# Kernel optimization log

Hardware: AMD Instinct MI355X
Metric: run time of the kernel (lower is better)

Reference implementation:

```python
import jax, jax.numpy as jnp
import numpy as np
from jax import lax

SCALE = 2
K_UP = 5
EPS = 1e-5
DN = ('NCHW', 'OIHW', 'NCHW')


def _bn(x, gamma, beta, mean, var):
    inv = gamma / jnp.sqrt(var + EPS)
    return x * inv[None, :, None, None] + (beta - mean * inv)[None, :, None, None]


def _pixel_shuffle(x, r):
    b, crr, h, w = x.shape
    c = crr // (r * r)
    x = x.reshape(b, c, r, r, h, w)
    x = x.transpose(0, 1, 4, 2, 5, 3)  # b, c, h, r, w, r
    return x.reshape(b, c, h * r, w * r)


def setup_inputs() -> dict:
    key = jax.random.key(0)
    ks = jax.random.split(key, 4)
    b, c, h, w = 4, 64, 128, 128
    c_mid = 64
    enc_out = (SCALE * K_UP) ** 2  # 100
    return {
        'X': jax.random.normal(ks[0], (b, c, h, w), jnp.float32),
        'comp_w': jax.random.normal(ks[1], (c_mid, c, 1, 1), jnp.float32) * 0.1,
        'comp_gamma': jnp.ones((c_mid,), jnp.float32),
        'comp_beta': jnp.zeros((c_mid,), jnp.float32),
        'comp_mean': jnp.zeros((c_mid,), jnp.float32),
        'comp_var': jnp.ones((c_mid,), jnp.float32),
        'enc_w': jax.random.normal(ks[2], (enc_out, c_mid, 3, 3), jnp.float32) * 0.05,
        'enc_b': jnp.zeros((enc_out,), jnp.float32),
        'enc_gamma': jnp.ones((enc_out,), jnp.float32),
        'enc_beta': jnp.zeros((enc_out,), jnp.float32),
        'enc_mean': jnp.zeros((enc_out,), jnp.float32),
        'enc_var': jnp.ones((enc_out,), jnp.float32),
    }


def reference(X, comp_w, comp_gamma, comp_beta, comp_mean, comp_var,
              enc_w, enc_b, enc_gamma, enc_beta, enc_mean, enc_var):
    b, c, h, w = X.shape
    h_, w_ = h * SCALE, w * SCALE
    # compress: 1x1 conv + BN + ReLU
    Wm = lax.conv_general_dilated(X, comp_w, (1, 1), 'VALID', dimension_numbers=DN)
    Wm = jax.nn.relu(_bn(Wm, comp_gamma, comp_beta, comp_mean, comp_var))
    # encode kernel weights: 3x3 conv + BN
    Wm = lax.conv_general_dilated(Wm, enc_w, (1, 1), ((1, 1), (1, 1)), dimension_numbers=DN)
    Wm = Wm + enc_b[None, :, None, None]
    Wm = _bn(Wm, enc_gamma, enc_beta, enc_mean, enc_var)
    # pixel shuffle -> [b, k_up^2, h_, w_], softmax over kernel dim
    Wm = _pixel_shuffle(Wm, SCALE)
    Wm = jax.nn.softmax(Wm, axis=1)
    # nearest upsample input
    Xu = jnp.repeat(jnp.repeat(X, SCALE, axis=2), SCALE, axis=3)  # [b,c,h_,w_]
    # unfold(k=5, dilation=2, pad=4) + einsum, fused as accumulation over the
    # 25 kernel taps (avoids the b*c*25*h_*w_ im2col blowup; identical math)
    pad = (K_UP // 2) * SCALE  # 4
    Xp = jnp.pad(Xu, ((0, 0), (0, 0), (pad, pad), (pad, pad)))
    out = jnp.zeros((b, c, h_, w_), X.dtype)
    for i in range(K_UP):
        for j in range(K_UP):
            k = i * K_UP + j
            patch = lax.dynamic_slice(Xp, (0, 0, i * SCALE, j * SCALE), (b, c, h_, w_))
            out = out + Wm[:, k:k + 1] * patch
    return out
```

## Files before the change

kernel.cpp:

```cpp
#include <hip/hip_runtime.h>

#define EPS 1e-5f

typedef __attribute__((ext_vector_type(8))) short short8;
typedef __attribute__((ext_vector_type(4))) float float4v;

__device__ inline unsigned short f2bf(float f) {
  unsigned u = __float_as_uint(f);
  unsigned r = (u + 0x7fffu + ((u >> 16) & 1u)) >> 16;
  return (unsigned short)r;
}
__device__ inline uint pk2(float a, float b) {
  return (uint)f2bf(a) | ((uint)f2bf(b) << 16);
}

__global__ __launch_bounds__(256) void xform_kernel(
    const float* __restrict__ enc_w, const float* __restrict__ enc_gamma,
    const float* __restrict__ enc_var, const float* __restrict__ comp_w,
    const float* __restrict__ comp_gamma, const float* __restrict__ comp_var,
    ushort* __restrict__ Awt, float* __restrict__ Wc) {
  int u = blockIdx.x * 256 + threadIdx.x;
  if (u < 9216) {
    int kc = u >> 9, rem = u & 511;
    int mt = rem >> 6, q = (rem >> 4) & 3, ml = rem & 15;
    int e = mt * 16 + ml;
    int t = kc >> 1, h = kc & 1;
    int dy = t / 3, dx = t - dy * 3;
    float inv = (e < 100) ? enc_gamma[e] * rsqrtf(enc_var[e] + EPS) : 0.f;
    ushort o[8];
#pragma unroll
    for (int j = 0; j < 8; ++j) {
      int ci = h * 32 + q * 8 + j;
      float w = (e < 100) ? enc_w[(e * 64 + ci) * 9 + dy * 3 + dx] * inv : 0.f;
      o[j] = f2bf(w);
    }
    uint4 v;
    v.x = (uint)o[0] | ((uint)o[1] << 16);
    v.y = (uint)o[2] | ((uint)o[3] << 16);
    v.z = (uint)o[4] | ((uint)o[5] << 16);
    v.w = (uint)o[6] | ((uint)o[7] << 16);
    *reinterpret_cast<uint4*>(Awt + (size_t)u * 8) = v;
  } else if (u < 9216 + 4096) {
    int v = u - 9216;
    int co = v & 63;
    float inv = comp_gamma[co] * rsqrtf(comp_var[co] + EPS);
    Wc[v] = comp_w[co * 64 + (v >> 6)] * inv;
  }
}

__global__ void bias_kernel(
    const float* __restrict__ enc_b, const float* __restrict__ enc_gamma,
    const float* __restrict__ enc_beta, const float* __restrict__ enc_mean,
    const float* __restrict__ enc_var, const float* __restrict__ comp_gamma,
    const float* __restrict__ comp_beta, const float* __restrict__ comp_mean,
    const float* __restrict__ comp_var, float* __restrict__ bias2,
    float* __restrict__ bias_c) {
  int t = threadIdx.x;
  if (t < 128) {
    float v = 0.f;
    if (t < 100) {
      float inv = enc_gamma[t] * rsqrtf(enc_var[t] + EPS);
      v = enc_b[t] * inv + enc_beta[t] - enc_mean[t] * inv;
    }
    bias2[t] = v;
  } else if (t < 192) {
    int c = t - 128;
    float inv = comp_gamma[c] * rsqrtf(comp_var[c] + EPS);
    bias_c[c] = comp_beta[c] - comp_mean[c] * inv;
  }
}

__global__ __launch_bounds__(256) void compress_kernel(
    const float* __restrict__ X, const float* __restrict__ Wc,
    const float* __restrict__ bias_c, ushort* __restrict__ out,
    ushort* __restrict__ Xb) {
  __shared__ __align__(16) float xtile[64 * 65];
  __shared__ __align__(16) float osm[64 * 68];
  const int tid = threadIdx.x;
  const int p0 = blockIdx.x * 64;
  const int b = p0 >> 14;
  const float* xbase = X + ((size_t)b << 20) + (p0 & 16383);

#pragma unroll
  for (int k = 0; k < 16; ++k) {
    int u = k * 256 + tid;
    int ci = u >> 6, px = u & 63;
    xtile[px * 65 + ci] = xbase[((size_t)ci << 14) + px];
  }
  __syncthreads();

  const int wv = __builtin_amdgcn_readfirstlane(tid >> 6);
  const int ln = tid & 63;
  float acc[16];
#pragma unroll
  for (int u = 0; u < 16; ++u) acc[u] = bias_c[wv * 16 + u];
  const float* xr = xtile + ln * 65;
#pragma unroll 8
  for (int ci = 0; ci < 64; ++ci) {
    float xv = xr[ci];
    const float* wr = Wc + ci * 64 + wv * 16;
#pragma unroll
    for (int u = 0; u < 16; ++u) acc[u] = fmaf(wr[u], xv, acc[u]);
  }
  float4v* orow = reinterpret_cast<float4v*>(osm) + ln * 17 + wv * 4;
#pragma unroll
  for (int j = 0; j < 4; ++j) {
    float4v t;
#pragma unroll
    for (int s = 0; s < 4; ++s) t[s] = fmaxf(acc[j * 4 + s], 0.f);
    orow[j] = t;
  }
  __syncthreads();

#pragma unroll
  for (int j = 0; j < 2; ++j) {
    int u = j * 256 + tid;
    int px = u >> 3, g = u & 7;
    const float* so = osm + px * 68 + g * 8;
    uint4 vo = make_uint4(pk2(so[0], so[1]), pk2(so[2], so[3]),
                          pk2(so[4], so[5]), pk2(so[6], so[7]));
    *reinterpret_cast<uint4*>(out + (size_t)(p0 + px) * 64 + g * 8) = vo;
    const float* sx = xtile + px * 65 + g * 8;
    uint4 vx = make_uint4(pk2(sx[0], sx[1]), pk2(sx[2], sx[3]),
                          pk2(sx[4], sx[5]), pk2(sx[6], sx[7]));
    *reinterpret_cast<uint4*>(Xb + (size_t)(p0 + px) * 64 + g * 8) = vx;
  }
}

__global__ __launch_bounds__(256) void encode_mfma(
    const ushort* __restrict__ Wm1t, const ushort* __restrict__ Awt,
    const float* __restrict__ bias2, uint* __restrict__ Wtu) {
  __shared__ __align__(16) char smem[25600];
  ushort* Xt = (ushort*)smem;
  const int tid = threadIdx.x;
  const int b = blockIdx.z;
  const int y0 = blockIdx.y * 8, x0 = blockIdx.x * 8;

  for (int u = tid; u < 800; u += 256) {
    int pos = u >> 3, cg = u & 7;
    int iy = pos / 10, ix = pos - iy * 10;
    int gy = y0 + iy - 1, gx = x0 + ix - 1;
    uint4 v = make_uint4(0, 0, 0, 0);
    if ((unsigned)gy < 128u && (unsigned)gx < 128u)
      v = *reinterpret_cast<const uint4*>(
          Wm1t + ((((size_t)b << 14) + (gy << 7) + gx) << 6) + cg * 8);
    *reinterpret_cast<uint4*>(&Xt[pos * 72 + cg * 8]) = v;
  }
  __syncthreads();

  const int wave = tid >> 6, lane = tid & 63;
  const int q = lane >> 4, px16 = lane & 15;

  float4v acc[2][4];
#pragma unroll
  for (int a = 0; a < 2; ++a)
#pragma unroll
    for (int n = 0; n < 4; ++n) acc[a][n] = (float4v){0.f, 0.f, 0.f, 0.f};

  const short8* Ap = reinterpret_cast<const short8*>(Awt);
#pragma unroll
  for (int kc = 0; kc < 18; ++kc) {
    const int t = kc >> 1, h = kc & 1;
    const int dy = t / 3, dx = t - dy * 3;
    short8 af[2];
#pragma unroll
    for (int a = 0; a < 2; ++a)
      af[a] = Ap[kc * 512 + (wave * 2 + a) * 64 + lane];
    short8 bfr[4];
#pragma unroll
    for (int n = 0; n < 4; ++n) {
      int p = n * 16 + px16;
      int iy = (p >> 3) + dy, ix = (p & 7) + dx;
      bfr[n] = *reinterpret_cast<const short8*>(
          &Xt[(iy * 10 + ix) * 72 + h * 32 + q * 8]);
    }
#pragma unroll
    for (int a = 0; a < 2; ++a)
#pragma unroll
      for (int n = 0; n < 4; ++n)
        acc[a][n] = __builtin_amdgcn_mfma_f32_16x16x32_bf16(
            af[a], bfr[n], acc[a][n], 0, 0, 0);
  }
  __syncthreads();

  float* wsm = (float*)smem;
#pragma unroll
  for (int a = 0; a < 2; ++a) {
    int ebase = (wave * 2 + a) * 16 + q * 4;
    if (ebase < 100) {
#pragma unroll
      for (int n = 0; n < 4; ++n) {
        int p = n * 16 + px16;
        *reinterpret_cast<float4v*>(wsm + p * 100 + ebase) = acc[a][n];
      }
    }
  }
  __syncthreads();

  if (tid < 64) {
    const float4v* bias4 = (const float4v*)bias2;
    float4v v[25];
    const float* wp = wsm + tid * 100;
#pragma unroll
    for (int j = 0; j < 25; ++j)
      v[j] = *reinterpret_cast<const float4v*>(wp + 4 * j) + bias4[j];
    float4v m = v[0];
#pragma unroll
    for (int j = 1; j < 25; ++j) {
      m.x = fmaxf(m.x, v[j].x); m.y = fmaxf(m.y, v[j].y);
      m.z = fmaxf(m.z, v[j].z); m.w = fmaxf(m.w, v[j].w);
    }
    float4v s = (float4v){0.f, 0.f, 0.f, 0.f};
#pragma unroll
    for (int j = 0; j < 25; ++j) {
      v[j].x = __expf(v[j].x - m.x); v[j].y = __expf(v[j].y - m.y);
      v[j].z = __expf(v[j].z - m.z); v[j].w = __expf(v[j].w - m.w);
      s += v[j];
    }
    float i0 = 1.f / s.x, i1 = 1.f / s.y, i2 = 1.f / s.z, i3 = 1.f / s.w;
    alignas(16) uint wp56[56];
#pragma unroll
    for (int k = 0; k < 25; ++k) {
      wp56[k]      = (uint)f2bf(v[k].x * i0) | ((uint)f2bf(v[k].y * i1) << 16);
      wp56[28 + k] = (uint)f2bf(v[k].z * i2) | ((uint)f2bf(v[k].w * i3) << 16);
    }
#pragma unroll
    for (int k = 25; k < 28; ++k) { wp56[k] = 0; wp56[28 + k] = 0; }
    int pix = b * 16384 + (y0 + (tid >> 3)) * 128 + x0 + (tid & 7);
    uint4* dst = reinterpret_cast<uint4*>(Wtu + (size_t)pix * 56);
#pragma unroll
    for (int j = 0; j < 14; ++j) dst[j] = reinterpret_cast<const uint4*>(wp56)[j];
  }
}

__global__ __launch_bounds__(256) void carafe_kernel(
    const ushort* __restrict__ Xb, const uint* __restrict__ Wtu,
    float* __restrict__ out) {
  const int tid = threadIdx.x;
  const int b = blockIdx.z;
  const int y0 = blockIdx.y * 8, x0 = blockIdx.x * 8;
  __shared__ __align__(16) ushort xt[144 * 72];

  for (int u = tid; u < 1152; u += 256) {
    int pos = u >> 3, cg = u & 7;
    int iy = pos / 12, ix = pos - iy * 12;
    int gy = y0 + iy - 2, gx = x0 + ix - 2;
    uint4 v = make_uint4(0, 0, 0, 0);
    if ((unsigned)gy < 128u && (unsigned)gx < 128u)
      v = *reinterpret_cast<const uint4*>(
          Xb + (((size_t)b * 16384 + gy * 128 + gx) << 6) + cg * 8);
    *reinterpret_cast<uint4*>(&xt[pos * 72 + cg * 8]) = v;
  }
  __syncthreads();

  const int p = tid & 63, q = tid >> 6;
  const int r1 = q & 1, cq = q >> 1;
  const int py = p >> 3, px = p & 7;

  int pix = b * 16384 + (y0 + py) * 128 + (x0 + px);
  const uint4* wq = reinterpret_cast<const uint4*>(Wtu + (size_t)pix * 56 + r1 * 28);
  alignas(16) uint w[28];
#pragma unroll
  for (int j = 0; j < 7; ++j) reinterpret_cast<uint4*>(w)[j] = wq[j];

  float2 acc[32];
#pragma unroll
  for (int i = 0; i < 32; ++i) acc[i] = make_float2(0.f, 0.f);

#pragma unroll
  for (int k = 0; k < 25; ++k) {
    const int dy = k / 5, dx = k - dy * 5;
    const ushort* bp = xt + ((py + dy) * 12 + (px + dx)) * 72 + cq * 32;
    float w0 = __uint_as_float(w[k] << 16);
    float w1 = __uint_as_float(w[k] & 0xffff0000u);
#pragma unroll
    for (int j = 0; j < 4; ++j) {
      uint4 xv = *reinterpret_cast<const uint4*>(bp + 8 * j);
      const uint xu[4] = {xv.x, xv.y, xv.z, xv.w};
#pragma unroll
      for (int t = 0; t < 4; ++t) {
        float xlo = __uint_as_float(xu[t] << 16);
        float xhi = __uint_as_float(xu[t] & 0xffff0000u);
        int c = j * 8 + t * 2;
        acc[c].x = fmaf(w0, xlo, acc[c].x);
        acc[c].y = fmaf(w1, xlo, acc[c].y);
        acc[c + 1].x = fmaf(w0, xhi, acc[c + 1].x);
        acc[c + 1].y = fmaf(w1, xhi, acc[c + 1].y);
      }
    }
  }

  int yq = (y0 + py) * 2 + r1;
  int xq = (x0 + px) * 2;
#pragma unroll
  for (int ci = 0; ci < 32; ++ci) {
    int c = cq * 32 + ci;
    *reinterpret_cast<float2*>(
        out + ((size_t)(b * 64 + c) * 256 + yq) * 256 + xq) = acc[ci];
  }
}

extern "C" void kernel_launch(void* const* d_in, const int* in_sizes, int n_in,
                              void* d_out, int out_size, void* d_ws, size_t ws_size,
                              hipStream_t stream) {
  const float* X          = (const float*)d_in[0];
  const float* comp_w     = (const float*)d_in[1];
  const float* comp_gamma = (const float*)d_in[2];
  const float* comp_beta  = (const float*)d_in[3];
  const float* comp_mean  = (const float*)d_in[4];
  const float* comp_var   = (const float*)d_in[5];
  const float* enc_w      = (const float*)d_in[6];
  const float* enc_b      = (const float*)d_in[7];
  const float* enc_gamma  = (const float*)d_in[8];
  const float* enc_beta   = (const float*)d_in[9];
  const float* enc_mean   = (const float*)d_in[10];
  const float* enc_var    = (const float*)d_in[11];
  float* out = (float*)d_out;

  char* ws = (char*)d_ws;
  ushort* Wm1t  = (ushort*)(ws);
  uint*   Wtu   = (uint*)(ws + 8388608);
  ushort* Xb    = (ushort*)(ws + 23068672);
  ushort* Awt   = (ushort*)(ws + 31457280);
  float*  Wc    = (float*)(ws + 31604736);
  float*  bias2 = (float*)(ws + 31621120);
  float*  biasc = (float*)(ws + 31621632);

  xform_kernel<<<52, 256, 0, stream>>>(enc_w, enc_gamma, enc_var,
                                       comp_w, comp_gamma, comp_var, Awt, Wc);
  bias_kernel<<<1, 256, 0, stream>>>(enc_b, enc_gamma, enc_beta, enc_mean,
                                     enc_var, comp_gamma, comp_beta, comp_mean,
                                     comp_var, bias2, biasc);
  compress_kernel<<<1024, 256, 0, stream>>>(X, Wc, biasc, Wm1t, Xb);
  encode_mfma<<<dim3(16, 16, 4), 256, 0, stream>>>(Wm1t, Awt, bias2, Wtu);
  carafe_kernel<<<dim3(16, 16, 4), 256, 0, stream>>>(Xb, Wtu, out);
}
```

Measured before the change: 148.1 us.

## Fuse encode and CARAFE kernels and merge bias setup into xform kernel

Merges the encoder MFMA kernel with the CARAFE reassembly kernel. Softmax weights now stay in shared memory instead of being written to and reread from a global buffer. The bias-computation kernel is folded into the weight-transform kernel, which removes a launch. In exchange, the fused kernel uses more shared memory (about 39 KB), which may lower occupancy, and the reassembly phase now runs behind the encode phase inside one block.

```diff
diff --git a/kernel.cpp b/kernel.cpp
--- a/kernel.cpp
+++ b/kernel.cpp
@@ -18,7 +18,11 @@
     const float* __restrict__ enc_w, const float* __restrict__ enc_gamma,
     const float* __restrict__ enc_var, const float* __restrict__ comp_w,
     const float* __restrict__ comp_gamma, const float* __restrict__ comp_var,
-    ushort* __restrict__ Awt, float* __restrict__ Wc) {
+    const float* __restrict__ enc_b, const float* __restrict__ enc_beta,
+    const float* __restrict__ enc_mean, const float* __restrict__ comp_beta,
+    const float* __restrict__ comp_mean, ushort* __restrict__ Awt,
+    float* __restrict__ Wc, float* __restrict__ bias2,
+    float* __restrict__ bias_c) {
   int u = blockIdx.x * 256 + threadIdx.x;
   if (u < 9216) {
     int kc = u >> 9, rem = u & 511;
@@ -40,31 +44,21 @@
     v.z = (uint)o[4] | ((uint)o[5] << 16);
     v.w = (uint)o[6] | ((uint)o[7] << 16);
     *reinterpret_cast<uint4*>(Awt + (size_t)u * 8) = v;
-  } else if (u < 9216 + 4096) {
+  } else if (u < 13312) {
     int v = u - 9216;
     int co = v & 63;
     float inv = comp_gamma[co] * rsqrtf(comp_var[co] + EPS);
     Wc[v] = comp_w[co * 64 + (v >> 6)] * inv;
-  }
-}
-
-__global__ void bias_kernel(
-    const float* __restrict__ enc_b, const float* __restrict__ enc_gamma,
-    const float* __restrict__ enc_beta, const float* __restrict__ enc_mean,
-    const float* __restrict__ enc_var, const float* __restrict__ comp_gamma,
-    const float* __restrict__ comp_beta, const float* __restrict__ comp_mean,
-    const float* __restrict__ comp_var, float* __restrict__ bias2,
-    float* __restrict__ bias_c) {
-  int t = threadIdx.x;
-  if (t < 128) {
+  } else if (u < 13440) {
+    int t = u - 13312;
     float v = 0.f;
     if (t < 100) {
       float inv = enc_gamma[t] * rsqrtf(enc_var[t] + EPS);
       v = enc_b[t] * inv + enc_beta[t] - enc_mean[t] * inv;
     }
     bias2[t] = v;
-  } else if (t < 192) {
-    int c = t - 128;
+  } else if (u < 13504) {
+    int c = u - 13440;
     float inv = comp_gamma[c] * rsqrtf(comp_var[c] + EPS);
     bias_c[c] = comp_beta[c] - comp_mean[c] * inv;
   }
@@ -127,10 +121,11 @@
   }
 }
 
-__global__ __launch_bounds__(256) void encode_mfma(
+__global__ __launch_bounds__(256) void encode_carafe(
     const ushort* __restrict__ Wm1t, const ushort* __restrict__ Awt,
-    const float* __restrict__ bias2, uint* __restrict__ Wtu) {
-  __shared__ __align__(16) char smem[25600];
+    const float* __restrict__ bias2, const ushort* __restrict__ Xb,
+    float* __restrict__ out) {
+  __shared__ __align__(16) char smem[39936];
   ushort* Xt = (ushort*)smem;
   const int tid = threadIdx.x;
   const int b = blockIdx.z;
@@ -197,6 +192,7 @@
   }
   __syncthreads();
 
+  uint* wpT = (uint*)(smem + 25600);
   if (tid < 64) {
     const float4v* bias4 = (const float4v*)bias2;
     float4v v[25];
@@ -218,29 +214,15 @@
       s += v[j];
     }
     float i0 = 1.f / s.x, i1 = 1.f / s.y, i2 = 1.f / s.z, i3 = 1.f / s.w;
-    alignas(16) uint wp56[56];
 #pragma unroll
     for (int k = 0; k < 25; ++k) {
-      wp56[k]      = (uint)f2bf(v[k].x * i0) | ((uint)f2bf(v[k].y * i1) << 16);
-      wp56[28 + k] = (uint)f2bf(v[k].z * i2) | ((uint)f2bf(v[k].w * i3) << 16);
-    }
-#pragma unroll
-    for (int k = 25; k < 28; ++k) { wp56[k] = 0; wp56[28 + k] = 0; }
-    int pix = b * 16384 + (y0 + (tid >> 3)) * 128 + x0 + (tid & 7);
-    uint4* dst = reinterpret_cast<uint4*>(Wtu + (size_t)pix * 56);
-#pragma unroll
-    for (int j = 0; j < 14; ++j) dst[j] = reinterpret_cast<const uint4*>(wp56)[j];
-  }
-}
-
-__global__ __launch_bounds__(256) void carafe_kernel(
-    const ushort* __restrict__ Xb, const uint* __restrict__ Wtu,
-    float* __restrict__ out) {
-  const int tid = threadIdx.x;
-  const int b = blockIdx.z;
-  const int y0 = blockIdx.y * 8, x0 = blockIdx.x * 8;
-  __shared__ __align__(16) ushort xt[144 * 72];
-
+      wpT[k * 64 + tid]        = pk2(v[k].x * i0, v[k].y * i1);
+      wpT[(28 + k) * 64 + tid] = pk2(v[k].z * i2, v[k].w * i3);
+    }
+  }
+  __syncthreads();
+
+  ushort* xt = (ushort*)smem;
   for (int u = tid; u < 1152; u += 256) {
     int pos = u >> 3, cg = u & 7;
     int iy = pos / 12, ix = pos - iy * 12;
@@ -253,50 +235,48 @@
   }
   __syncthreads();
 
-  const int p = tid & 63, q = tid >> 6;
-  const int r1 = q & 1, cq = q >> 1;
-  const int py = p >> 3, px = p & 7;
-
-  int pix = b * 16384 + (y0 + py) * 128 + (x0 + px);
-  const uint4* wq = reinterpret_cast<const uint4*>(Wtu + (size_t)pix * 56 + r1 * 28);
-  alignas(16) uint w[28];
-#pragma unroll
-  for (int j = 0; j < 7; ++j) reinterpret_cast<uint4*>(w)[j] = wq[j];
-
-  float2 acc[32];
-#pragma unroll
-  for (int i = 0; i < 32; ++i) acc[i] = make_float2(0.f, 0.f);
-
-#pragma unroll
-  for (int k = 0; k < 25; ++k) {
-    const int dy = k / 5, dx = k - dy * 5;
-    const ushort* bp = xt + ((py + dy) * 12 + (px + dx)) * 72 + cq * 32;
-    float w0 = __uint_as_float(w[k] << 16);
-    float w1 = __uint_as_float(w[k] & 0xffff0000u);
-#pragma unroll
-    for (int j = 0; j < 4; ++j) {
-      uint4 xv = *reinterpret_cast<const uint4*>(bp + 8 * j);
-      const uint xu[4] = {xv.x, xv.y, xv.z, xv.w};
-#pragma unroll
-      for (int t = 0; t < 4; ++t) {
-        float xlo = __uint_as_float(xu[t] << 16);
-        float xhi = __uint_as_float(xu[t] & 0xffff0000u);
-        int c = j * 8 + t * 2;
-        acc[c].x = fmaf(w0, xlo, acc[c].x);
-        acc[c].y = fmaf(w1, xlo, acc[c].y);
-        acc[c + 1].x = fmaf(w0, xhi, acc[c + 1].x);
-        acc[c + 1].y = fmaf(w1, xhi, acc[c + 1].y);
+  {
+    const int p = tid & 63, qq = tid >> 6;
+    const int r1 = qq & 1, cq = qq >> 1;
+    const int py = p >> 3, pxl = p & 7;
+    const uint* wrow = wpT + r1 * 28 * 64 + p;
+
+    float2 acc2[32];
+#pragma unroll
+    for (int i = 0; i < 32; ++i) acc2[i] = make_float2(0.f, 0.f);
+
+#pragma unroll
+    for (int k = 0; k < 25; ++k) {
+      const int dy = k / 5, dx = k - dy * 5;
+      const ushort* bp = xt + ((py + dy) * 12 + (pxl + dx)) * 72 + cq * 32;
+      uint wk = wrow[k * 64];
+      float w0 = __uint_as_float(wk << 16);
+      float w1 = __uint_as_float(wk & 0xffff0000u);
+#pragma unroll
+      for (int j = 0; j < 4; ++j) {
+        uint4 xv = *reinterpret_cast<const uint4*>(bp + 8 * j);
+        const uint xu[4] = {xv.x, xv.y, xv.z, xv.w};
+#pragma unroll
+        for (int t = 0; t < 4; ++t) {
+          float xlo = __uint_as_float(xu[t] << 16);
+          float xhi = __uint_as_float(xu[t] & 0xffff0000u);
+          int c = j * 8 + t * 2;
+          acc2[c].x = fmaf(w0, xlo, acc2[c].x);
+          acc2[c].y = fmaf(w1, xlo, acc2[c].y);
+          acc2[c + 1].x = fmaf(w0, xhi, acc2[c + 1].x);
+          acc2[c + 1].y = fmaf(w1, xhi, acc2[c + 1].y);
+        }
       }
     }
-  }
-
-  int yq = (y0 + py) * 2 + r1;
-  int xq = (x0 + px) * 2;
-#pragma unroll
-  for (int ci = 0; ci < 32; ++ci) {
-    int c = cq * 32 + ci;
-    *reinterpret_cast<float2*>(
-        out + ((size_t)(b * 64 + c) * 256 + yq) * 256 + xq) = acc[ci];
+
+    int yq = (y0 + py) * 2 + r1;
+    int xq = (x0 + pxl) * 2;
+#pragma unroll
+    for (int ci = 0; ci < 32; ++ci) {
+      int c = cq * 32 + ci;
+      *reinterpret_cast<float2*>(
+          out + ((size_t)(b * 64 + c) * 256 + yq) * 256 + xq) = acc2[ci];
+    }
   }
 }
 
@@ -319,19 +299,17 @@
 
   char* ws = (char*)d_ws;
   ushort* Wm1t  = (ushort*)(ws);
-  uint*   Wtu   = (uint*)(ws + 8388608);
-  ushort* Xb    = (ushort*)(ws + 23068672);
-  ushort* Awt   = (ushort*)(ws + 31457280);
-  float*  Wc    = (float*)(ws + 31604736);
-  float*  bias2 = (float*)(ws + 31621120);
-  float*  biasc = (float*)(ws + 31621632);
-
-  xform_kernel<<<52, 256, 0, stream>>>(enc_w, enc_gamma, enc_var,
-                                       comp_w, comp_gamma, comp_var, Awt, Wc);
-  bias_kernel<<<1, 256, 0, stream>>>(enc_b, enc_gamma, enc_beta, enc_mean,
-                                     enc_var, comp_gamma, comp_beta, comp_mean,
-                                     comp_var, bias2, biasc);
+  ushort* Xb    = (ushort*)(ws + 8388608);
+  ushort* Awt   = (ushort*)(ws + 16777216);
+  float*  Wc    = (float*)(ws + 16924672);
+  float*  bias2 = (float*)(ws + 16941056);
+  float*  biasc = (float*)(ws + 16941568);
+
+  xform_kernel<<<53, 256, 0, stream>>>(enc_w, enc_gamma, enc_var,
+                                       comp_w, comp_gamma, comp_var,
+                                       enc_b, enc_beta, enc_mean,
+                                       comp_beta, comp_mean,
+                                       Awt, Wc, bias2, biasc);
   compress_kernel<<<1024, 256, 0, stream>>>(X, Wc, biasc, Wm1t, Xb);
-  encode_mfma<<<dim3(16, 16, 4), 256, 0, stream>>>(Wm1t, Awt, bias2, Wtu);
-  carafe_kernel<<<dim3(16, 16, 4), 256, 0, stream>>>(Xb, Wtu, out);
-}
+  encode_carafe<<<dim3(16, 16, 4), 256, 0, stream>>>(Wm1t, Awt, bias2, Xb, out);
+}
```

After: 170.7 us. 1.15x slower.
